# Optimization experiments

Measured on AMD Instinct MI355X. Metric: run time of the kernel, lower is better.

The kernel has to match this reference:

```python
import jax, jax.numpy as jnp
import numpy as np

W, M, N, K = 8, 4096, 4096, 1792  # world_size, tokens, d_model, per-rank K shard


def setup_inputs() -> dict:
    key = jax.random.key(0)
    k1, k2 = jax.random.split(key)
    # Per-rank activations and per-rank weight shards (row-parallel linear).
    inp = jax.random.normal(k1, (W, M, K), dtype=jnp.float32) * 0.05
    wgt = jax.random.normal(k2, (W, N, K), dtype=jnp.float32) * 0.05
    return {"input": inp, "weight": wgt}


def reference(input, weight):
    # Per rank r: partial_r = input_r @ weight_r.T  -> [M, N]
    # All-reduce (sum over ranks) fused into the contraction.
    return jnp.einsum("rmk,rnk->mn", input, weight)
```

## Files before the change

### kernel.cpp

```cpp
#include <hip/hip_runtime.h>
#include <hip/hip_bf16.h>


#define Wsz 8
#define Mdim 4096
#define Ndim 4096
#define Kshard 1792
#define KTOT 14336
#define LDSBUF 32768

typedef __attribute__((ext_vector_type(8))) short short8;
typedef __attribute__((ext_vector_type(4))) float f32x4;

__device__ __forceinline__ unsigned short f2bf(float x) {
    unsigned u = __builtin_bit_cast(unsigned, x);
    u = (u + 0x7FFFu + ((u >> 16) & 1u)) >> 16;
    return (unsigned short)u;
}

__global__ void __launch_bounds__(256) cvt_kernel(const float* __restrict__ src,
                                                  unsigned short* __restrict__ dst) {
    unsigned g = blockIdx.x * 256 + threadIdx.x;
    unsigned k8 = g % 224u;
    unsigned t  = g / 224u;
    unsigned m  = t & 4095u;
    unsigned r  = t >> 12;
    const float4* p = (const float4*)(src + ((size_t)r * Mdim * Kshard + (size_t)m * Kshard + k8 * 8));
    float4 v0 = p[0], v1 = p[1];
    uint4 o;
    o.x = (unsigned)f2bf(v0.x) | ((unsigned)f2bf(v0.y) << 16);
    o.y = (unsigned)f2bf(v0.z) | ((unsigned)f2bf(v0.w) << 16);
    o.z = (unsigned)f2bf(v1.x) | ((unsigned)f2bf(v1.y) << 16);
    o.w = (unsigned)f2bf(v1.z) | ((unsigned)f2bf(v1.w) << 16);
    *(uint4*)(dst + ((size_t)m * KTOT + (size_t)r * Kshard + k8 * 8)) = o;
}

__global__ void __launch_bounds__(512, 2) gemm_bt(const unsigned short* __restrict__ A,
                                                  const unsigned short* __restrict__ B,
                                                  float* __restrict__ C) {
    extern __shared__ char smem[];

    const int tid = threadIdx.x;
    const int w = tid >> 6, lane = tid & 63;
    const int l15 = lane & 15, quad = lane >> 4;
    const int wm = (w >> 1) * 64;
    const int wn = (w & 1) * 128;
    const long bm = (long)blockIdx.y * 256, bn = (long)blockIdx.x * 256;

    const int chunk = w * 64 + lane;
    const int sr = chunk >> 2;
    const int sq = (chunk & 3) ^ ((sr >> 1) & 3);
    const unsigned short* aP0 = A + (size_t)(bm + sr) * KTOT + sq * 8;
    const unsigned short* aP1 = aP0 + (size_t)128 * KTOT;
    const unsigned short* bP0 = B + (size_t)(bn + sr) * KTOT + sq * 8;
    const unsigned short* bP1 = bP0 + (size_t)128 * KTOT;
    const int ldsW = w * 1024;

    const int swz = (quad ^ ((l15 >> 1) & 3)) * 16;
    const int aoff = (wm + l15) * 64 + swz;
    const int boff = 16384 + (wn + l15) * 64 + swz;

    f32x4 acc[4][8] = {};

#define STAGE(bufbase, kt)                                                                              \
    do {                                                                                                \
        __builtin_amdgcn_global_load_lds((const __attribute__((address_space(1))) void*)(aP0 + (kt)),   \
            (__attribute__((address_space(3))) void*)(smem + (bufbase) + ldsW), 16, 0, 0);              \
        __builtin_amdgcn_global_load_lds((const __attribute__((address_space(1))) void*)(aP1 + (kt)),   \
            (__attribute__((address_space(3))) void*)(smem + (bufbase) + ldsW + 8192), 16, 0, 0);       \
        __builtin_amdgcn_global_load_lds((const __attribute__((address_space(1))) void*)(bP0 + (kt)),   \
            (__attribute__((address_space(3))) void*)(smem + (bufbase) + 16384 + ldsW), 16, 0, 0);      \
        __builtin_amdgcn_global_load_lds((const __attribute__((address_space(1))) void*)(bP1 + (kt)),   \
            (__attribute__((address_space(3))) void*)(smem + (bufbase) + 16384 + ldsW + 8192), 16, 0, 0);\
    } while (0)

#define COMPUTE(bufbase)                                                                 \
    do {                                                                                 \
        short8 af[4], bfr[8];                                                            \
        _Pragma("unroll") for (int i = 0; i < 4; ++i)                                    \
            af[i] = *(const short8*)(smem + (bufbase) + aoff + i * 1024);                \
        _Pragma("unroll") for (int i = 0; i < 8; ++i)                                    \
            bfr[i] = *(const short8*)(smem + (bufbase) + boff + i * 1024);               \
        _Pragma("unroll") for (int mi = 0; mi < 4; ++mi)                                 \
            _Pragma("unroll") for (int ni = 0; ni < 8; ++ni)                             \
                acc[mi][ni] = __builtin_amdgcn_mfma_f32_16x16x32_bf16(af[mi], bfr[ni],   \
                                                                      acc[mi][ni], 0, 0, 0); \
    } while (0)

#define PIPE_BAR4() asm volatile("s_waitcnt vmcnt(4)\ns_barrier" ::: "memory")
#define PIPE_BAR0() asm volatile("s_waitcnt vmcnt(0)\ns_barrier" ::: "memory")

    STAGE(0, 0);
    STAGE(LDSBUF, 32);

    long kt = 0;
    for (int blk = 0; blk < 111; ++blk) {
#pragma unroll
        for (int u = 0; u < 4; ++u) {
            PIPE_BAR4();
            STAGE(((u + 2) & 3) * LDSBUF, kt + 64);
            COMPUTE(u * LDSBUF);
            kt += 32;
        }
    }
    PIPE_BAR4(); STAGE(2 * LDSBUF, kt + 64); COMPUTE(0);          kt += 32;
    PIPE_BAR4(); STAGE(3 * LDSBUF, kt + 64); COMPUTE(LDSBUF);     kt += 32;
    PIPE_BAR4();                             COMPUTE(2 * LDSBUF);
    PIPE_BAR0();                             COMPUTE(3 * LDSBUF);

#undef STAGE
#undef COMPUTE
#undef PIPE_BAR4
#undef PIPE_BAR0

#pragma unroll
    for (int mi = 0; mi < 4; ++mi)
#pragma unroll
        for (int ni = 0; ni < 8; ++ni) {
            const long col = bn + wn + ni * 16 + l15;
#pragma unroll
            for (int r2 = 0; r2 < 4; ++r2) {
                const long row = bm + wm + mi * 16 + quad * 4 + r2;
                C[row * Ndim + col] = acc[mi][ni][r2];
            }
        }
}

__global__ void __launch_bounds__(256) gemm_inline(const float* __restrict__ A,
                                                   const float* __restrict__ B,
                                                   float* __restrict__ C) {
    __shared__ short As[128 * 32];
    __shared__ short Bs[128 * 32];

    const int tid = threadIdx.x;
    const int w = tid >> 6, lane = tid & 63;
    const int bm = blockIdx.y * 128, bn = blockIdx.x * 128;
    const int wm = (w >> 1) * 64, wn = (w & 1) * 64;
    const int lane15 = lane & 15, quad = lane >> 4;

    const int srow = tid >> 3;
    const int skc  = (tid & 7) * 4;

    const char* a_rd = (const char*)As + ((size_t)(wm + lane15) * 32 + quad * 8) * 2;
    const char* b_rd = (const char*)Bs + ((size_t)(wn + lane15) * 32 + quad * 8) * 2;

    f32x4 acc[4][4] = {};
    long base = 0; int kloc = 0;

    for (int kt = 0; kt < KTOT; kt += 32) {
        const float* ap = A + base + kloc + (long)(bm + srow) * Kshard + skc;
        const float* bp = B + base + kloc + (long)(bn + srow) * Kshard + skc;
        float4 av[4], bv[4];
#pragma unroll
        for (int i = 0; i < 4; ++i) {
            av[i] = *(const float4*)(ap + (long)i * 32 * Kshard);
            bv[i] = *(const float4*)(bp + (long)i * 32 * Kshard);
        }
        __syncthreads();
#pragma unroll
        for (int i = 0; i < 4; ++i) {
            ushort4 oa, ob;
            oa.x = f2bf(av[i].x); oa.y = f2bf(av[i].y); oa.z = f2bf(av[i].z); oa.w = f2bf(av[i].w);
            ob.x = f2bf(bv[i].x); ob.y = f2bf(bv[i].y); ob.z = f2bf(bv[i].z); ob.w = f2bf(bv[i].w);
            *(ushort4*)((char*)As + ((size_t)(srow + i * 32) * 32 + skc) * 2) = oa;
            *(ushort4*)((char*)Bs + ((size_t)(srow + i * 32) * 32 + skc) * 2) = ob;
        }
        __syncthreads();

        short8 af[4], bfr[4];
#pragma unroll
        for (int i = 0; i < 4; ++i) {
            af[i]  = *(const short8*)(a_rd + (size_t)i * 16 * 64);
            bfr[i] = *(const short8*)(b_rd + (size_t)i * 16 * 64);
        }
#pragma unroll
        for (int mi = 0; mi < 4; ++mi)
#pragma unroll
            for (int ni = 0; ni < 4; ++ni)
                acc[mi][ni] = __builtin_amdgcn_mfma_f32_16x16x32_bf16(af[mi], bfr[ni], acc[mi][ni], 0, 0, 0);

        kloc += 32;
        if (kloc == Kshard) { kloc = 0; base += (long)Mdim * Kshard; }
    }

#pragma unroll
    for (int mi = 0; mi < 4; ++mi)
#pragma unroll
        for (int ni = 0; ni < 4; ++ni) {
            const int col = bn + wn + ni * 16 + lane15;
#pragma unroll
            for (int r2 = 0; r2 < 4; ++r2) {
                const int row = bm + wm + mi * 16 + quad * 4 + r2;
                C[(size_t)row * Ndim + col] = acc[mi][ni][r2];
            }
        }
}

extern "C" void kernel_launch(void* const* d_in, const int* in_sizes, int n_in,
                              void* d_out, int out_size, void* d_ws, size_t ws_size,
                              hipStream_t stream) {
    const float* inp = (const float*)d_in[0];
    const float* wgt = (const float*)d_in[1];
    float* out = (float*)d_out;

    const size_t one_mat = (size_t)Mdim * KTOT * 2;
    if (ws_size >= 2 * one_mat) {
        unsigned short* Abf = (unsigned short*)d_ws;
        unsigned short* Bbf = (unsigned short*)((char*)d_ws + one_mat);
        const int cvt_blocks = (Wsz * Mdim * (Kshard / 8)) / 256;
        cvt_kernel<<<cvt_blocks, 256, 0, stream>>>(inp, Abf);
        cvt_kernel<<<cvt_blocks, 256, 0, stream>>>(wgt, Bbf);
        hipFuncSetAttribute(reinterpret_cast<const void*>(gemm_bt),
                            hipFuncAttributeMaxDynamicSharedMemorySize, 4 * LDSBUF);
        dim3 grid(Ndim / 256, Mdim / 256);
        gemm_bt<<<grid, 512, 4 * LDSBUF, stream>>>(Abf, Bbf, out);
    } else {
        dim3 grid(Ndim / 128, Mdim / 128);
        gemm_inline<<<grid, 256, 0, stream>>>(inp, wgt, out);
    }
}
```

Before: 869.0 us.

## Split GEMM k-step into two MFMA phases with barriers, priority hints; fuse conversion kernels

The two fp32-to-bf16 conversion launches become one kernel that covers both inputs, with each thread converting two float4 chunks into uint2 stores. The GEMM inner step is restructured into two halves: it loads A and half of B fragments, issues the next async stage, barriers, and runs 16 MFMAs at raised wave priority. It then loads the second B half and runs the remaining 16 MFMAs, and the wait-and-barrier moves to the tail of each step. This is meant to interleave LDS reads, global-to-LDS loads and MFMA work more tightly across waves, at the cost of extra barriers per k-step.

```diff
diff --git a/kernel.cpp b/kernel.cpp
--- a/kernel.cpp
+++ b/kernel.cpp
@@ -18,21 +18,30 @@
     return (unsigned short)u;
 }
 
-__global__ void __launch_bounds__(256) cvt_kernel(const float* __restrict__ src,
-                                                  unsigned short* __restrict__ dst) {
-    unsigned g = blockIdx.x * 256 + threadIdx.x;
-    unsigned k8 = g % 224u;
-    unsigned t  = g / 224u;
-    unsigned m  = t & 4095u;
-    unsigned r  = t >> 12;
-    const float4* p = (const float4*)(src + ((size_t)r * Mdim * Kshard + (size_t)m * Kshard + k8 * 8));
-    float4 v0 = p[0], v1 = p[1];
-    uint4 o;
-    o.x = (unsigned)f2bf(v0.x) | ((unsigned)f2bf(v0.y) << 16);
-    o.y = (unsigned)f2bf(v0.z) | ((unsigned)f2bf(v0.w) << 16);
-    o.z = (unsigned)f2bf(v1.x) | ((unsigned)f2bf(v1.y) << 16);
-    o.w = (unsigned)f2bf(v1.z) | ((unsigned)f2bf(v1.w) << 16);
-    *(uint4*)(dst + ((size_t)m * KTOT + (size_t)r * Kshard + k8 * 8)) = o;
+__global__ void __launch_bounds__(256) cvt2_kernel(const float* __restrict__ s0,
+                                                   const float* __restrict__ s1,
+                                                   unsigned short* __restrict__ d0,
+                                                   unsigned short* __restrict__ d1) {
+    const unsigned BPM = (Wsz * Mdim * (Kshard / 4)) / 512;
+    unsigned b = blockIdx.x;
+    const float* src;
+    unsigned short* dst;
+    if (b >= BPM) { src = s1; dst = d1; b -= BPM; }
+    else          { src = s0; dst = d0; }
+    const unsigned f0 = b * 512 + threadIdx.x;
+#pragma unroll
+    for (int i = 0; i < 2; ++i) {
+        const unsigned f  = f0 + i * 256;
+        const unsigned k4 = f % 448u;
+        const unsigned t  = f / 448u;
+        const unsigned m  = t & 4095u;
+        const unsigned r  = t >> 12;
+        const float4 v = ((const float4*)src)[f];
+        uint2 o;
+        o.x = (unsigned)f2bf(v.x) | ((unsigned)f2bf(v.y) << 16);
+        o.y = (unsigned)f2bf(v.z) | ((unsigned)f2bf(v.w) << 16);
+        ((uint2*)dst)[(size_t)m * (KTOT / 4) + r * (Kshard / 4) + k4] = o;
+    }
 }
 
 __global__ void __launch_bounds__(512, 2) gemm_bt(const unsigned short* __restrict__ A,
@@ -74,44 +83,59 @@
             (__attribute__((address_space(3))) void*)(smem + (bufbase) + 16384 + ldsW + 8192), 16, 0, 0);\
     } while (0)
 
-#define COMPUTE(bufbase)                                                                 \
+#define KSTEP(bufbase, DOSTAGE, stagebase, kt, TAILASM)                                  \
     do {                                                                                 \
-        short8 af[4], bfr[8];                                                            \
+        short8 af[4], bf0[4], bf1[4];                                                    \
         _Pragma("unroll") for (int i = 0; i < 4; ++i)                                    \
             af[i] = *(const short8*)(smem + (bufbase) + aoff + i * 1024);                \
-        _Pragma("unroll") for (int i = 0; i < 8; ++i)                                    \
-            bfr[i] = *(const short8*)(smem + (bufbase) + boff + i * 1024);               \
+        _Pragma("unroll") for (int i = 0; i < 4; ++i)                                    \
+            bf0[i] = *(const short8*)(smem + (bufbase) + boff + i * 1024);               \
+        if (DOSTAGE) STAGE(stagebase, kt);                                               \
+        asm volatile("s_barrier" ::: "memory");                                          \
+        __builtin_amdgcn_sched_barrier(0);                                               \
+        __builtin_amdgcn_s_setprio(1);                                                   \
         _Pragma("unroll") for (int mi = 0; mi < 4; ++mi)                                 \
-            _Pragma("unroll") for (int ni = 0; ni < 8; ++ni)                             \
-                acc[mi][ni] = __builtin_amdgcn_mfma_f32_16x16x32_bf16(af[mi], bfr[ni],   \
+            _Pragma("unroll") for (int ni = 0; ni < 4; ++ni)                             \
+                acc[mi][ni] = __builtin_amdgcn_mfma_f32_16x16x32_bf16(af[mi], bf0[ni],   \
                                                                       acc[mi][ni], 0, 0, 0); \
+        __builtin_amdgcn_s_setprio(0);                                                   \
+        _Pragma("unroll") for (int i = 0; i < 4; ++i)                                    \
+            bf1[i] = *(const short8*)(smem + (bufbase) + boff + (4 + i) * 1024);         \
+        asm volatile("s_barrier" ::: "memory");                                          \
+        __builtin_amdgcn_sched_barrier(0);                                               \
+        __builtin_amdgcn_s_setprio(1);                                                   \
+        _Pragma("unroll") for (int mi = 0; mi < 4; ++mi)                                 \
+            _Pragma("unroll") for (int ni = 0; ni < 4; ++ni)                             \
+                acc[mi][ni + 4] = __builtin_amdgcn_mfma_f32_16x16x32_bf16(af[mi], bf1[ni], \
+                                                                      acc[mi][ni + 4], 0, 0, 0); \
+        __builtin_amdgcn_s_setprio(0);                                                   \
+        asm volatile(TAILASM ::: "memory");                                              \
     } while (0)
 
-#define PIPE_BAR4() asm volatile("s_waitcnt vmcnt(4)\ns_barrier" ::: "memory")
-#define PIPE_BAR0() asm volatile("s_waitcnt vmcnt(0)\ns_barrier" ::: "memory")
+#define TAIL4 "s_waitcnt vmcnt(4)\ns_barrier"
+#define TAIL0 "s_waitcnt vmcnt(0)\ns_barrier"
 
     STAGE(0, 0);
     STAGE(LDSBUF, 32);
+    asm volatile(TAIL4 ::: "memory");
 
     long kt = 0;
     for (int blk = 0; blk < 111; ++blk) {
 #pragma unroll
         for (int u = 0; u < 4; ++u) {
-            PIPE_BAR4();
-            STAGE(((u + 2) & 3) * LDSBUF, kt + 64);
-            COMPUTE(u * LDSBUF);
+            KSTEP(u * LDSBUF, true, ((u + 2) & 3) * LDSBUF, kt + 64, TAIL4);
             kt += 32;
         }
     }
-    PIPE_BAR4(); STAGE(2 * LDSBUF, kt + 64); COMPUTE(0);          kt += 32;
-    PIPE_BAR4(); STAGE(3 * LDSBUF, kt + 64); COMPUTE(LDSBUF);     kt += 32;
-    PIPE_BAR4();                             COMPUTE(2 * LDSBUF);
-    PIPE_BAR0();                             COMPUTE(3 * LDSBUF);
+    KSTEP(0,          true,  2 * LDSBUF, kt + 64, TAIL4); kt += 32;
+    KSTEP(LDSBUF,     true,  3 * LDSBUF, kt + 64, TAIL4); kt += 32;
+    KSTEP(2 * LDSBUF, false, 0,          0,       TAIL0);
+    KSTEP(3 * LDSBUF, false, 0,          0,       "");
 
 #undef STAGE
-#undef COMPUTE
-#undef PIPE_BAR4
-#undef PIPE_BAR0
+#undef KSTEP
+#undef TAIL4
+#undef TAIL0
 
 #pragma unroll
     for (int mi = 0; mi < 4; ++mi)
@@ -207,9 +231,8 @@
     if (ws_size >= 2 * one_mat) {
         unsigned short* Abf = (unsigned short*)d_ws;
         unsigned short* Bbf = (unsigned short*)((char*)d_ws + one_mat);
-        const int cvt_blocks = (Wsz * Mdim * (Kshard / 8)) / 256;
-        cvt_kernel<<<cvt_blocks, 256, 0, stream>>>(inp, Abf);
-        cvt_kernel<<<cvt_blocks, 256, 0, stream>>>(wgt, Bbf);
+        const int cvt_blocks = 2 * ((Wsz * Mdim * (Kshard / 4)) / 512);
+        cvt2_kernel<<<cvt_blocks, 256, 0, stream>>>(inp, wgt, Abf, Bbf);
         hipFuncSetAttribute(reinterpret_cast<const void*>(gemm_bt),
                             hipFuncAttributeMaxDynamicSharedMemorySize, 4 * LDSBUF);
         dim3 grid(Ndim / 256, Mdim / 256);
```

New measurement: 907.7 us. 1.04x slower.

## Fuse fp32-to-bf16 conversion into GEMM register-staged double-buffered pipeline

Applied to the files above, without the earlier changes.

Removes the separate conversion kernels and bf16 workspace. The GEMM now loads fp32 tiles straight from the per-rank inputs into registers, converts them with packed bf16 conversion instructions, and writes them to a two-buffer LDS pipeline. The grid is flattened and remapped so concurrently running blocks share rows. This drops a full extra read and write pass over both operands, but the GEMM now reads twice as many bytes per tile and uses more registers for staging. The async global-to-LDS loads and the four-stage buffering are given up.

```diff
diff --git a/kernel.cpp b/kernel.cpp
--- a/kernel.cpp
+++ b/kernel.cpp
@@ -8,36 +8,16 @@
 #define Kshard 1792
 #define KTOT 14336
 #define LDSBUF 32768
+#define MK ((size_t)Mdim * Kshard)
 
 typedef __attribute__((ext_vector_type(8))) short short8;
 typedef __attribute__((ext_vector_type(4))) float f32x4;
 
-__device__ __forceinline__ unsigned short f2bf(float x) {
-    unsigned u = __builtin_bit_cast(unsigned, x);
-    u = (u + 0x7FFFu + ((u >> 16) & 1u)) >> 16;
-    return (unsigned short)u;
-}
+struct Stage { float4 a0l, a0h, a1l, a1h, b0l, b0h, b1l, b1h; };
 
-__global__ void __launch_bounds__(256) cvt_kernel(const float* __restrict__ src,
-                                                  unsigned short* __restrict__ dst) {
-    unsigned g = blockIdx.x * 256 + threadIdx.x;
-    unsigned k8 = g % 224u;
-    unsigned t  = g / 224u;
-    unsigned m  = t & 4095u;
-    unsigned r  = t >> 12;
-    const float4* p = (const float4*)(src + ((size_t)r * Mdim * Kshard + (size_t)m * Kshard + k8 * 8));
-    float4 v0 = p[0], v1 = p[1];
-    uint4 o;
-    o.x = (unsigned)f2bf(v0.x) | ((unsigned)f2bf(v0.y) << 16);
-    o.y = (unsigned)f2bf(v0.z) | ((unsigned)f2bf(v0.w) << 16);
-    o.z = (unsigned)f2bf(v1.x) | ((unsigned)f2bf(v1.y) << 16);
-    o.w = (unsigned)f2bf(v1.z) | ((unsigned)f2bf(v1.w) << 16);
-    *(uint4*)(dst + ((size_t)m * KTOT + (size_t)r * Kshard + k8 * 8)) = o;
-}
-
-__global__ void __launch_bounds__(512, 2) gemm_bt(const unsigned short* __restrict__ A,
-                                                  const unsigned short* __restrict__ B,
-                                                  float* __restrict__ C) {
+__global__ void __launch_bounds__(512, 2) gemm_fused(const float* __restrict__ A,
+                                                     const float* __restrict__ B,
+                                                     float* __restrict__ C) {
     extern __shared__ char smem[];
 
     const int tid = threadIdx.x;
@@ -45,16 +25,18 @@
     const int l15 = lane & 15, quad = lane >> 4;
     const int wm = (w >> 1) * 64;
     const int wn = (w & 1) * 128;
-    const long bm = (long)blockIdx.y * 256, bn = (long)blockIdx.x * 256;
 
-    const int chunk = w * 64 + lane;
-    const int sr = chunk >> 2;
-    const int sq = (chunk & 3) ^ ((sr >> 1) & 3);
-    const unsigned short* aP0 = A + (size_t)(bm + sr) * KTOT + sq * 8;
-    const unsigned short* aP1 = aP0 + (size_t)128 * KTOT;
-    const unsigned short* bP0 = B + (size_t)(bn + sr) * KTOT + sq * 8;
-    const unsigned short* bP1 = bP0 + (size_t)128 * KTOT;
-    const int ldsW = w * 1024;
+    const int wgid = (blockIdx.x & 7) * 32 + (blockIdx.x >> 3);
+    const long bm = (long)(wgid >> 4) * 256, bn = (long)(wgid & 15) * 256;
+
+    const int g = w * 64 + lane;
+    const int sr = g >> 2;
+    const int sq = (g & 3) ^ ((sr >> 1) & 3);
+    const float* aRow0 = A + (size_t)(bm + sr) * Kshard + sq * 8;
+    const float* aRow1 = aRow0 + (size_t)128 * Kshard;
+    const float* bRow0 = B + (size_t)(bn + sr) * Kshard + sq * 8;
+    const float* bRow1 = bRow0 + (size_t)128 * Kshard;
+    const int ldsWr = g * 16;
 
     const int swz = (quad ^ ((l15 >> 1) & 3)) * 16;
     const int aoff = (wm + l15) * 64 + swz;
@@ -62,16 +44,37 @@
 
     f32x4 acc[4][8] = {};
 
-#define STAGE(bufbase, kt)                                                                              \
-    do {                                                                                                \
-        __builtin_amdgcn_global_load_lds((const __attribute__((address_space(1))) void*)(aP0 + (kt)),   \
-            (__attribute__((address_space(3))) void*)(smem + (bufbase) + ldsW), 16, 0, 0);              \
-        __builtin_amdgcn_global_load_lds((const __attribute__((address_space(1))) void*)(aP1 + (kt)),   \
-            (__attribute__((address_space(3))) void*)(smem + (bufbase) + ldsW + 8192), 16, 0, 0);       \
-        __builtin_amdgcn_global_load_lds((const __attribute__((address_space(1))) void*)(bP0 + (kt)),   \
-            (__attribute__((address_space(3))) void*)(smem + (bufbase) + 16384 + ldsW), 16, 0, 0);      \
-        __builtin_amdgcn_global_load_lds((const __attribute__((address_space(1))) void*)(bP1 + (kt)),   \
-            (__attribute__((address_space(3))) void*)(smem + (bufbase) + 16384 + ldsW + 8192), 16, 0, 0);\
+#define ISSUE(S, off)                                           \
+    do {                                                        \
+        S.a0l = *(const float4*)(aRow0 + (off));                \
+        S.a0h = *(const float4*)(aRow0 + (off) + 4);            \
+        S.a1l = *(const float4*)(aRow1 + (off));                \
+        S.a1h = *(const float4*)(aRow1 + (off) + 4);            \
+        S.b0l = *(const float4*)(bRow0 + (off));                \
+        S.b0h = *(const float4*)(bRow0 + (off) + 4);            \
+        S.b1l = *(const float4*)(bRow1 + (off));                \
+        S.b1h = *(const float4*)(bRow1 + (off) + 4);            \
+    } while (0)
+
+#define CV4(dst, lo, hi)                                                          \
+    do {                                                                          \
+        asm("v_cvt_pk_bf16_f32 %0, %1, %2" : "=v"(dst.x) : "v"(lo.x), "v"(lo.y)); \
+        asm("v_cvt_pk_bf16_f32 %0, %1, %2" : "=v"(dst.y) : "v"(lo.z), "v"(lo.w)); \
+        asm("v_cvt_pk_bf16_f32 %0, %1, %2" : "=v"(dst.z) : "v"(hi.x), "v"(hi.y)); \
+        asm("v_cvt_pk_bf16_f32 %0, %1, %2" : "=v"(dst.w) : "v"(hi.z), "v"(hi.w)); \
+    } while (0)
+
+#define CONVWRITE(S, base)                                      \
+    do {                                                        \
+        uint4 oA0, oA1, oB0, oB1;                               \
+        CV4(oA0, S.a0l, S.a0h);                                 \
+        CV4(oA1, S.a1l, S.a1h);                                 \
+        CV4(oB0, S.b0l, S.b0h);                                 \
+        CV4(oB1, S.b1l, S.b1h);                                 \
+        *(uint4*)(smem + (base) + ldsWr) = oA0;                 \
+        *(uint4*)(smem + (base) + 8192 + ldsWr) = oA1;          \
+        *(uint4*)(smem + (base) + 16384 + ldsWr) = oB0;         \
+        *(uint4*)(smem + (base) + 24576 + ldsWr) = oB1;         \
     } while (0)
 
 #define COMPUTE(bufbase)                                                                 \
@@ -87,31 +90,63 @@
                                                                       acc[mi][ni], 0, 0, 0); \
     } while (0)
 
-#define PIPE_BAR4() asm volatile("s_waitcnt vmcnt(4)\ns_barrier" ::: "memory")
-#define PIPE_BAR0() asm volatile("s_waitcnt vmcnt(0)\ns_barrier" ::: "memory")
+#define ADV() do { kkI += 32; if (kkI == Kshard) { kkI = 0; baseI += MK; } } while (0)
+#define SB() __builtin_amdgcn_sched_barrier(0)
+#define WAIT_VM8() asm volatile("s_waitcnt vmcnt(8)" ::: "memory")
+#define WAIT_VM0() asm volatile("s_waitcnt vmcnt(0)" ::: "memory")
+#define ENDSTEP()  asm volatile("s_waitcnt lgkmcnt(0)\ns_barrier" ::: "memory")
 
-    STAGE(0, 0);
-    STAGE(LDSBUF, 32);
+    Stage S0, S1;
+    size_t baseI = 0;
+    int kkI = 32;
 
-    long kt = 0;
-    for (int blk = 0; blk < 111; ++blk) {
-#pragma unroll
-        for (int u = 0; u < 4; ++u) {
-            PIPE_BAR4();
-            STAGE(((u + 2) & 3) * LDSBUF, kt + 64);
-            COMPUTE(u * LDSBUF);
-            kt += 32;
-        }
+    ISSUE(S0, 0);
+    ISSUE(S1, 32);
+    WAIT_VM8(); SB();
+    CONVWRITE(S0, 0);
+    ENDSTEP(); SB();
+
+    for (int blk = 0; blk < 222; ++blk) {
+        ADV(); ISSUE(S0, baseI + kkI); SB();
+        COMPUTE(0);
+        WAIT_VM8(); SB();
+        CONVWRITE(S1, LDSBUF);
+        ENDSTEP(); SB();
+        ADV(); ISSUE(S1, baseI + kkI); SB();
+        COMPUTE(LDSBUF);
+        WAIT_VM8(); SB();
+        CONVWRITE(S0, 0);
+        ENDSTEP(); SB();
     }
-    PIPE_BAR4(); STAGE(2 * LDSBUF, kt + 64); COMPUTE(0);          kt += 32;
-    PIPE_BAR4(); STAGE(3 * LDSBUF, kt + 64); COMPUTE(LDSBUF);     kt += 32;
-    PIPE_BAR4();                             COMPUTE(2 * LDSBUF);
-    PIPE_BAR0();                             COMPUTE(3 * LDSBUF);
 
-#undef STAGE
+    ADV(); ISSUE(S0, baseI + kkI); SB();
+    COMPUTE(0);
+    WAIT_VM8(); SB();
+    CONVWRITE(S1, LDSBUF);
+    ENDSTEP(); SB();
+
+    ADV(); ISSUE(S1, baseI + kkI); SB();
+    COMPUTE(LDSBUF);
+    WAIT_VM8(); SB();
+    CONVWRITE(S0, 0);
+    ENDSTEP(); SB();
+
+    COMPUTE(0);
+    WAIT_VM0(); SB();
+    CONVWRITE(S1, LDSBUF);
+    ENDSTEP(); SB();
+
+    COMPUTE(LDSBUF);
+
+#undef ISSUE
+#undef CV4
+#undef CONVWRITE
 #undef COMPUTE
-#undef PIPE_BAR4
-#undef PIPE_BAR0
+#undef ADV
+#undef SB
+#undef WAIT_VM8
+#undef WAIT_VM0
+#undef ENDSTEP
 
 #pragma unroll
     for (int mi = 0; mi < 4; ++mi)
@@ -126,76 +161,6 @@
         }
 }
 
-__global__ void __launch_bounds__(256) gemm_inline(const float* __restrict__ A,
-                                                   const float* __restrict__ B,
-                                                   float* __restrict__ C) {
-    __shared__ short As[128 * 32];
-    __shared__ short Bs[128 * 32];
-
-    const int tid = threadIdx.x;
-    const int w = tid >> 6, lane = tid & 63;
-    const int bm = blockIdx.y * 128, bn = blockIdx.x * 128;
-    const int wm = (w >> 1) * 64, wn = (w & 1) * 64;
-    const int lane15 = lane & 15, quad = lane >> 4;
-
-    const int srow = tid >> 3;
-    const int skc  = (tid & 7) * 4;
-
-    const char* a_rd = (const char*)As + ((size_t)(wm + lane15) * 32 + quad * 8) * 2;
-    const char* b_rd = (const char*)Bs + ((size_t)(wn + lane15) * 32 + quad * 8) * 2;
-
-    f32x4 acc[4][4] = {};
-    long base = 0; int kloc = 0;
-
-    for (int kt = 0; kt < KTOT; kt += 32) {
-        const float* ap = A + base + kloc + (long)(bm + srow) * Kshard + skc;
-        const float* bp = B + base + kloc + (long)(bn + srow) * Kshard + skc;
-        float4 av[4], bv[4];
-#pragma unroll
-        for (int i = 0; i < 4; ++i) {
-            av[i] = *(const float4*)(ap + (long)i * 32 * Kshard);
-            bv[i] = *(const float4*)(bp + (long)i * 32 * Kshard);
-        }
-        __syncthreads();
-#pragma unroll
-        for (int i = 0; i < 4; ++i) {
-            ushort4 oa, ob;
-            oa.x = f2bf(av[i].x); oa.y = f2bf(av[i].y); oa.z = f2bf(av[i].z); oa.w = f2bf(av[i].w);
-            ob.x = f2bf(bv[i].x); ob.y = f2bf(bv[i].y); ob.z = f2bf(bv[i].z); ob.w = f2bf(bv[i].w);
-            *(ushort4*)((char*)As + ((size_t)(srow + i * 32) * 32 + skc) * 2) = oa;
-            *(ushort4*)((char*)Bs + ((size_t)(srow + i * 32) * 32 + skc) * 2) = ob;
-        }
-        __syncthreads();
-
-        short8 af[4], bfr[4];
-#pragma unroll
-        for (int i = 0; i < 4; ++i) {
-            af[i]  = *(const short8*)(a_rd + (size_t)i * 16 * 64);
-            bfr[i] = *(const short8*)(b_rd + (size_t)i * 16 * 64);
-        }
-#pragma unroll
-        for (int mi = 0; mi < 4; ++mi)
-#pragma unroll
-            for (int ni = 0; ni < 4; ++ni)
-                acc[mi][ni] = __builtin_amdgcn_mfma_f32_16x16x32_bf16(af[mi], bfr[ni], acc[mi][ni], 0, 0, 0);
-
-        kloc += 32;
-        if (kloc == Kshard) { kloc = 0; base += (long)Mdim * Kshard; }
-    }
-
-#pragma unroll
-    for (int mi = 0; mi < 4; ++mi)
-#pragma unroll
-        for (int ni = 0; ni < 4; ++ni) {
-            const int col = bn + wn + ni * 16 + lane15;
-#pragma unroll
-            for (int r2 = 0; r2 < 4; ++r2) {
-                const int row = bm + wm + mi * 16 + quad * 4 + r2;
-                C[(size_t)row * Ndim + col] = acc[mi][ni][r2];
-            }
-        }
-}
-
 extern "C" void kernel_launch(void* const* d_in, const int* in_sizes, int n_in,
                               void* d_out, int out_size, void* d_ws, size_t ws_size,
                               hipStream_t stream) {
@@ -203,19 +168,7 @@
     const float* wgt = (const float*)d_in[1];
     float* out = (float*)d_out;
 
-    const size_t one_mat = (size_t)Mdim * KTOT * 2;
-    if (ws_size >= 2 * one_mat) {
-        unsigned short* Abf = (unsigned short*)d_ws;
-        unsigned short* Bbf = (unsigned short*)((char*)d_ws + one_mat);
-        const int cvt_blocks = (Wsz * Mdim * (Kshard / 8)) / 256;
-        cvt_kernel<<<cvt_blocks, 256, 0, stream>>>(inp, Abf);
-        cvt_kernel<<<cvt_blocks, 256, 0, stream>>>(wgt, Bbf);
-        hipFuncSetAttribute(reinterpret_cast<const void*>(gemm_bt),
-                            hipFuncAttributeMaxDynamicSharedMemorySize, 4 * LDSBUF);
-        dim3 grid(Ndim / 256, Mdim / 256);
-        gemm_bt<<<grid, 512, 4 * LDSBUF, stream>>>(Abf, Bbf, out);
-    } else {
-        dim3 grid(Ndim / 128, Mdim / 128);
-        gemm_inline<<<grid, 256, 0, stream>>>(inp, wgt, out);
-    }
+    hipFuncSetAttribute(reinterpret_cast<const void*>(gemm_fused),
+                        hipFuncAttributeMaxDynamicSharedMemorySize, 2 * LDSBUF);
+    gemm_fused<<<256, 512, 2 * LDSBUF, stream>>>(inp, wgt, out);
 }
```

Result: slower. 912.9 us (+5.0%).
